# Optimization experiments

Measured on AMD Instinct MI355X. Metric: run time of the kernel, lower is better.

Reference implementation:

```python
import jax, jax.numpy as jnp
import numpy as np


def setup_inputs() -> dict:
    key = jax.random.key(0)
    k1, k2 = jax.random.split(key)
    x = jax.random.normal(k1, (16, 4096, 3), dtype=jnp.float32)  # [B, N, 3]
    y = jax.random.normal(k2, (16, 4096, 3), dtype=jnp.float32)  # [B, M, 3]
    return {"x": x, "y": y}


def reference(x, y):
    # Squared pairwise distances via the ||x||^2 + ||y||^2 - 2<x,y> expansion.
    # d: [B, N, M]
    x2 = jnp.sum(x * x, axis=-1)  # [B, N]
    y2 = jnp.sum(y * y, axis=-1)  # [B, M]
    xy = jnp.einsum('bnd,bmd->bnm', x, y)  # [B, N, M]
    d = x2[:, :, None] + y2[:, None, :] - 2.0 * xy
    # directed Chamfer terms: mean over own points of min sq-dist to other cloud
    dist_to_y = jnp.mean(jnp.min(d, axis=2), axis=1)  # [B] (x -> y)
    dist_to_x = jnp.mean(jnp.min(d, axis=1), axis=1)  # [B] (y -> x)
    # per-cloud max of the two directed distances, averaged over batch
    return jnp.mean(jnp.maximum(dist_to_y, dist_to_x))
```

## Files before the change

kernel.cpp:

```cpp
#include <hip/hip_runtime.h>


typedef __attribute__((ext_vector_type(8)))  short bf16x8;
typedef __attribute__((ext_vector_type(16))) float f32x16;

#define BATCH   16
#define NPTS    4096
#define DB      (2 * BATCH)
#define GM_F32  (2 * DB * NPTS)

static __device__ __forceinline__ unsigned bf16rn(float f) {
  unsigned u = __float_as_uint(f);
  return (u + 0x7FFFu + ((u >> 16) & 1u)) >> 16;
}
static __device__ __forceinline__ float bf2f(unsigned h) {
  return __uint_as_float(h << 16);
}
static __device__ __forceinline__ unsigned pk(unsigned lo, unsigned hi) {
  return (lo & 0xFFFFu) | (hi << 16);
}

__global__ __launch_bounds__(512) void chamfer_mm(
    const float* __restrict__ x, const float* __restrict__ y,
    float* __restrict__ gm, unsigned* __restrict__ cnt) {
  __shared__ __align__(16) uint4 afl[64 * 64];

  const int bid = blockIdx.x;
  const int tid = threadIdx.x;
  if (bid == 0 && tid == 0) *cnt = 0;

  const int db  = bid >> 4;
  const int r   = bid & 15;
  const int c   = r >> 1;
  const int h   = r & 1;
  const int dir = db >> 4, b = db & 15;
  const float* own   = (dir == 0 ? x : y) + (size_t)b * NPTS * 3;
  const float* other = (dir == 0 ? y : x) + (size_t)b * NPTS * 3;
  const float* mp    = other + (size_t)h * 2048 * 3;

  #pragma unroll
  for (int k = 0; k < 4; ++k) {
    const int p = tid + k * 512;
    float y0 = mp[p * 3 + 0], y1 = mp[p * 3 + 1], y2 = mp[p * 3 + 2];
    float wv = fmaf(y2, y2, fmaf(y1, y1, y0 * y0));
    float z0 = -2.f * y0, z1 = -2.f * y1, z2 = -2.f * y2;
    unsigned h0 = bf16rn(z0), h1 = bf16rn(z1), h2 = bf16rn(z2);
    unsigned e0 = bf16rn(z0 - bf2f(h0));
    unsigned e1 = bf16rn(z1 - bf2f(h1));
    unsigned e2 = bf16rn(z2 - bf2f(h2));
    unsigned wh = bf16rn(wv), wl = bf16rn(wv - bf2f(wh));
    const int tile = p >> 5, row = p & 31;
    afl[tile * 64 + row]      =
        make_uint4(pk(h0, h1), pk(h2, e0), pk(e1, e2), pk(h0, h1));
    afl[tile * 64 + 32 + row] =
        make_uint4(pk(h2, wh), pk(wl, 0u), 0u, 0u);
  }

  const int w = tid >> 6, l = tid & 63;
  const int col = l & 31, kh = l >> 5;
  const unsigned ONE = 0x3F80u;
  bf16x8 bfr[2];
  float sq[2], rmn[2];
  #pragma unroll
  for (int nt = 0; nt < 2; ++nt) {
    const int n = c * 512 + w * 64 + nt * 32 + col;
    float a0 = own[n * 3 + 0], a1 = own[n * 3 + 1], a2 = own[n * 3 + 2];
    sq[nt]  = fmaf(a2, a2, fmaf(a1, a1, a0 * a0));
    rmn[nt] = 1e30f;
    unsigned h0 = bf16rn(a0), h1 = bf16rn(a1), h2 = bf16rn(a2);
    unsigned e0 = bf16rn(a0 - bf2f(h0));
    unsigned e1 = bf16rn(a1 - bf2f(h1));
    unsigned e2 = bf16rn(a2 - bf2f(h2));
    union { unsigned uu[4]; bf16x8 v; } U;
    U.uu[0] = (kh == 0) ? pk(h0, h1) : pk(e2, ONE);
    U.uu[1] = (kh == 0) ? pk(h2, h0) : pk(ONE, 0u);
    U.uu[2] = (kh == 0) ? pk(h1, h2) : 0u;
    U.uu[3] = (kh == 0) ? pk(e0, e1) : 0u;
    bfr[nt] = U.v;
  }
  __syncthreads();

  const int aoff = kh * 32 + col;
  const f32x16 z16 = {0.f, 0.f, 0.f, 0.f, 0.f, 0.f, 0.f, 0.f,
                      0.f, 0.f, 0.f, 0.f, 0.f, 0.f, 0.f, 0.f};
  #pragma unroll 4
  for (int mt = 0; mt < 64; ++mt) {
    union { uint4 u; bf16x8 v; } A;
    A.u = afl[mt * 64 + aoff];
    #pragma unroll
    for (int nt = 0; nt < 2; ++nt) {
      f32x16 acc = __builtin_amdgcn_mfma_f32_32x32x16_bf16(
          A.v, bfr[nt], z16, 0, 0, 0);
      float m0 = fminf(fminf(acc[0],  acc[1]),  acc[2]);
      float m1 = fminf(fminf(acc[3],  acc[4]),  acc[5]);
      float m2 = fminf(fminf(acc[6],  acc[7]),  acc[8]);
      float m3 = fminf(fminf(acc[9],  acc[10]), acc[11]);
      float m4 = fminf(fminf(acc[12], acc[13]), acc[14]);
      float m5 = fminf(fminf(acc[15], m0), m1);
      float m6 = fminf(fminf(m2, m3), m4);
      rmn[nt] = fminf(fminf(m5, m6), rmn[nt]);
    }
  }

  #pragma unroll
  for (int nt = 0; nt < 2; ++nt) {
    float v = fminf(rmn[nt], __shfl_xor(rmn[nt], 32, 64));
    float sv = v + sq[nt];
    if (l < 32)
      gm[(size_t)(h * DB + db) * NPTS + c * 512 + w * 64 + nt * 32 + col] = sv;
  }
}

__global__ __launch_bounds__(256) void chamfer_combine(
    const float* __restrict__ gm, float* __restrict__ dist,
    unsigned* __restrict__ cnt, float* __restrict__ out) {
  const int db = blockIdx.x;
  const float* g0 = gm + (size_t)db * NPTS;
  const float* g1 = gm + (size_t)(DB + db) * NPTS;
  float s = 0.0f;
  for (int i = threadIdx.x; i < NPTS; i += 256)
    s += fminf(g0[i], g1[i]);
  #pragma unroll
  for (int off = 32; off > 0; off >>= 1) s += __shfl_down(s, off, 64);
  __shared__ float red[4];
  const int lane = threadIdx.x & 63, wid = threadIdx.x >> 6;
  if (lane == 0) red[wid] = s;
  __syncthreads();
  if (threadIdx.x == 0) {
    dist[db] = ((red[0] + red[1]) + (red[2] + red[3])) * (1.0f / (float)NPTS);
    __threadfence();
    unsigned old = __hip_atomic_fetch_add(cnt, 1u, __ATOMIC_ACQ_REL,
                                          __HIP_MEMORY_SCOPE_AGENT);
    if (old == DB - 1) {
      __threadfence();
      float acc = 0.0f;
      #pragma unroll
      for (int b = 0; b < BATCH; ++b) {
        float d0 = __uint_as_float(__hip_atomic_load(
            (const unsigned*)&dist[b], __ATOMIC_RELAXED,
            __HIP_MEMORY_SCOPE_AGENT));
        float d1 = __uint_as_float(__hip_atomic_load(
            (const unsigned*)&dist[b + BATCH], __ATOMIC_RELAXED,
            __HIP_MEMORY_SCOPE_AGENT));
        acc += fmaxf(d0, d1);
      }
      out[0] = acc * (1.0f / (float)BATCH);
    }
  }
}

extern "C" void kernel_launch(void* const* d_in, const int* in_sizes, int n_in,
                              void* d_out, int out_size, void* d_ws, size_t ws_size,
                              hipStream_t stream) {
  const float* x = (const float*)d_in[0];
  const float* y = (const float*)d_in[1];
  float* out = (float*)d_out;

  float* gm     = (float*)d_ws;
  float* dist   = gm + GM_F32;
  unsigned* cnt = (unsigned*)(dist + DB);

  chamfer_mm<<<512, 512, 0, stream>>>(x, y, gm, cnt);
  chamfer_combine<<<DB, 256, 0, stream>>>(gm, dist, cnt, out);
}
```

Baseline: 29.77 us.

## Fuse combine kernel into main kernel via last-block atomic counters

Removes the separate combine kernel launch. Each of the 32 direction-batch groups now counts finished blocks with an atomic, and the last of its 16 blocks reduces that group's per-point minima into dist. A global counter then lets the last group finish the batch mean. A hipMemsetAsync is added to zero the counters, which brings back a separate stream operation, and the tail work is serialized onto single blocks.

```diff
diff --git a/kernel.cpp b/kernel.cpp
--- a/kernel.cpp
+++ b/kernel.cpp
@@ -22,12 +22,15 @@
 
 __global__ __launch_bounds__(512) void chamfer_mm(
     const float* __restrict__ x, const float* __restrict__ y,
-    float* __restrict__ gm, unsigned* __restrict__ cnt) {
+    float* __restrict__ gm, float* __restrict__ dist,
+    unsigned* __restrict__ dbcnt, unsigned* __restrict__ gcnt,
+    float* __restrict__ out) {
   __shared__ __align__(16) uint4 afl[64 * 64];
+  __shared__ float red2[8];
+  __shared__ int amLastDb, amLastAll;
 
   const int bid = blockIdx.x;
   const int tid = threadIdx.x;
-  if (bid == 0 && tid == 0) *cnt = 0;
 
   const int db  = bid >> 4;
   const int r   = bid & 15;
@@ -109,42 +112,56 @@
     if (l < 32)
       gm[(size_t)(h * DB + db) * NPTS + c * 512 + w * 64 + nt * 32 + col] = sv;
   }
-}
 
-__global__ __launch_bounds__(256) void chamfer_combine(
-    const float* __restrict__ gm, float* __restrict__ dist,
-    unsigned* __restrict__ cnt, float* __restrict__ out) {
-  const int db = blockIdx.x;
-  const float* g0 = gm + (size_t)db * NPTS;
-  const float* g1 = gm + (size_t)(DB + db) * NPTS;
-  float s = 0.0f;
-  for (int i = threadIdx.x; i < NPTS; i += 256)
-    s += fminf(g0[i], g1[i]);
-  #pragma unroll
-  for (int off = 32; off > 0; off >>= 1) s += __shfl_down(s, off, 64);
-  __shared__ float red[4];
-  const int lane = threadIdx.x & 63, wid = threadIdx.x >> 6;
-  if (lane == 0) red[wid] = s;
+  if (tid == 0) {
+    __threadfence();
+    unsigned old = __hip_atomic_fetch_add(&dbcnt[db], 1u, __ATOMIC_ACQ_REL,
+                                          __HIP_MEMORY_SCOPE_AGENT);
+    amLastDb = (old == 15);
+  }
   __syncthreads();
-  if (threadIdx.x == 0) {
-    dist[db] = ((red[0] + red[1]) + (red[2] + red[3])) * (1.0f / (float)NPTS);
+  if (amLastDb) {
     __threadfence();
-    unsigned old = __hip_atomic_fetch_add(cnt, 1u, __ATOMIC_ACQ_REL,
-                                          __HIP_MEMORY_SCOPE_AGENT);
-    if (old == DB - 1) {
+    const unsigned* g0 = (const unsigned*)(gm + (size_t)db * NPTS);
+    const unsigned* g1 = (const unsigned*)(gm + (size_t)(DB + db) * NPTS);
+    float s = 0.0f;
+    #pragma unroll
+    for (int i = tid; i < NPTS; i += 512) {
+      float v0 = __uint_as_float(__hip_atomic_load(
+          &g0[i], __ATOMIC_RELAXED, __HIP_MEMORY_SCOPE_AGENT));
+      float v1 = __uint_as_float(__hip_atomic_load(
+          &g1[i], __ATOMIC_RELAXED, __HIP_MEMORY_SCOPE_AGENT));
+      s += fminf(v0, v1);
+    }
+    #pragma unroll
+    for (int off = 32; off > 0; off >>= 1) s += __shfl_down(s, off, 64);
+    if (l == 0) red2[w] = s;
+    __syncthreads();
+    if (tid == 0) {
+      float t = 0.0f;
+      #pragma unroll
+      for (int k2 = 0; k2 < 8; ++k2) t += red2[k2];
+      dist[db] = t * (1.0f / (float)NPTS);
       __threadfence();
-      float acc = 0.0f;
-      #pragma unroll
-      for (int b = 0; b < BATCH; ++b) {
+      unsigned o2 = __hip_atomic_fetch_add(gcnt, 1u, __ATOMIC_ACQ_REL,
+                                           __HIP_MEMORY_SCOPE_AGENT);
+      amLastAll = (o2 == DB - 1);
+    }
+    __syncthreads();
+    if (amLastAll) {
+      __threadfence();
+      if (tid < BATCH) {
         float d0 = __uint_as_float(__hip_atomic_load(
-            (const unsigned*)&dist[b], __ATOMIC_RELAXED,
+            (const unsigned*)&dist[tid], __ATOMIC_RELAXED,
             __HIP_MEMORY_SCOPE_AGENT));
         float d1 = __uint_as_float(__hip_atomic_load(
-            (const unsigned*)&dist[b + BATCH], __ATOMIC_RELAXED,
+            (const unsigned*)&dist[tid + BATCH], __ATOMIC_RELAXED,
             __HIP_MEMORY_SCOPE_AGENT));
-        acc += fmaxf(d0, d1);
+        float mx = fmaxf(d0, d1);
+        #pragma unroll
+        for (int off = 8; off > 0; off >>= 1) mx += __shfl_down(mx, off, 16);
+        if (tid == 0) out[0] = mx * (1.0f / (float)BATCH);
       }
-      out[0] = acc * (1.0f / (float)BATCH);
     }
   }
 }
@@ -156,10 +173,11 @@
   const float* y = (const float*)d_in[1];
   float* out = (float*)d_out;
 
-  float* gm     = (float*)d_ws;
-  float* dist   = gm + GM_F32;
-  unsigned* cnt = (unsigned*)(dist + DB);
+  float* gm       = (float*)d_ws;
+  float* dist     = gm + GM_F32;
+  unsigned* dbcnt = (unsigned*)(dist + DB);
+  unsigned* gcnt  = dbcnt + DB;
 
-  chamfer_mm<<<512, 512, 0, stream>>>(x, y, gm, cnt);
-  chamfer_combine<<<DB, 256, 0, stream>>>(gm, dist, cnt, out);
+  hipMemsetAsync(dbcnt, 0, (DB + 1) * sizeof(unsigned), stream);
+  chamfer_mm<<<512, 512, 0, stream>>>(x, y, gm, dist, dbcnt, gcnt, out);
 }
```

After: 68.19 us. +129.0%, slower.
